# Kernel tuning notes

Measured on AMD Instinct MI355X. Metric: run time of the kernel, lower is better.

## Reference

```python
import jax, jax.numpy as jnp
import numpy as np

B, S, D, H = 4, 2048, 1024, 16
DH = D // H


def setup_inputs() -> dict:
    key = jax.random.key(0)
    ks = jax.random.split(key, 5)
    std = 1.0 / np.sqrt(D)
    return {
        "x": jax.random.normal(ks[0], (B, S, D), dtype=jnp.float32),
        "mask": jnp.ones((S, S), dtype=bool),  # unused by the original forward
        "Wq": jax.random.normal(ks[1], (D, D), dtype=jnp.float32) * std,
        "Wk": jax.random.normal(ks[2], (D, D), dtype=jnp.float32) * std,
        "Wv": jax.random.normal(ks[3], (D, D), dtype=jnp.float32) * std,
        "Wout": jax.random.normal(ks[4], (D, D), dtype=jnp.float32) * std,
    }


def reference(x, mask, Wq, Wk, Wv, Wout):
    n, s, d = x.shape
    scale = 1.0 / np.sqrt(DH).astype(np.float32)
    q = (x @ Wq).reshape(n, s, H, DH)
    k = (x @ Wk).reshape(n, s, H, DH)
    v = (x @ Wv).reshape(n, s, H, DH)
    # scores [n, q, k, h]; softmax over k axis (dim=-2 in original)
    attn = jnp.einsum('nqhd,nkhd->nqkh', q, k) * scale
    attn = jax.nn.softmax(attn, axis=-2)
    z = jnp.einsum('nqkh,nkhd->nqhd', attn, v).reshape(n, s, d)
    z = jnp.einsum('nqd,de->nqe', z, Wout)
    return x + z
```

## Files before the change

### kernel.cpp

```cpp
#include <hip/hip_runtime.h>

#define Bn 4
#define Sn 2048
#define Dn 1024
#define Hn 16
#define DHn 64

typedef float f32x4 __attribute__((ext_vector_type(4)));
typedef short bf16x8 __attribute__((ext_vector_type(8)));
typedef unsigned short u16;
typedef unsigned int u32;
typedef unsigned short u16x8 __attribute__((ext_vector_type(8)));
typedef unsigned short u16x4 __attribute__((ext_vector_type(4)));
typedef u32 u32x4 __attribute__((ext_vector_type(4)));

union B8 { u32x4 u; bf16x8 s; u16x8 h; };

__device__ __forceinline__ u16 f2bf(float f){
  union { float f; u32 u; } v; v.f = f;
  return (u16)((v.u + 0x7fffu + ((v.u >> 16) & 1u)) >> 16);
}

__device__ __forceinline__ u32 pack_bf2(float lo, float hi){
  union { float f; u32 u; } a, b;
  a.f = lo; b.f = hi;
  return __builtin_amdgcn_perm(b.u, a.u, 0x07060302u);
}

#if __has_builtin(__builtin_amdgcn_exp2f)
#define EXP2(x) __builtin_amdgcn_exp2f(x)
#define QSCALE 0.18033688011112042f
#else
#define EXP2(x) __expf(x)
#define QSCALE 0.125f
#endif

#if __has_builtin(__builtin_amdgcn_global_load_lds)
#define G2L16(l, g) __builtin_amdgcn_global_load_lds((const __attribute__((address_space(1))) u32*)(g), \
                                                     (__attribute__((address_space(3))) u32*)(l), 16, 0, 0)
#else
#define G2L16(l, g) (*(bf16x8*)(l) = *(const bf16x8*)(g))
#endif

#define MFMA_B16(d, va, vb) (d) = __builtin_amdgcn_mfma_f32_16x16x32_bf16((va), (vb), (d), 0, 0, 0)
#define BARRAW() __builtin_amdgcn_s_barrier()
#define WAIT_LGKM0() asm volatile("s_waitcnt lgkmcnt(0)" ::: "memory")
#define VM4() asm volatile("s_waitcnt vmcnt(4)" ::: "memory")
#define VM0() asm volatile("s_waitcnt vmcnt(0)" ::: "memory")
#define SCHEDB() __builtin_amdgcn_sched_barrier(0)

__global__ void prep_kernel(const float* __restrict__ x,
                            const float* __restrict__ Wq, const float* __restrict__ Wk,
                            const float* __restrict__ Wv, const float* __restrict__ Wo,
                            u16* __restrict__ xb, u16* __restrict__ wt_all){
  __shared__ u16 tile[64*66];
  const int t = threadIdx.x;
  if (blockIdx.x < 4096){
    size_t i = ((size_t)blockIdx.x * 256 + t) * 8;
    float4 f0 = *(const float4*)(x + i);
    float4 f1 = *(const float4*)(x + i + 4);
    u16x8 o;
    o[0]=f2bf(f0.x); o[1]=f2bf(f0.y); o[2]=f2bf(f0.z); o[3]=f2bf(f0.w);
    o[4]=f2bf(f1.x); o[5]=f2bf(f1.y); o[6]=f2bf(f1.z); o[7]=f2bf(f1.w);
    *(u16x8*)(xb + i) = o;
    return;
  }
  const int wi = blockIdx.x - 4096;
  const int z = wi >> 8, r8 = wi & 255;
  const int k0 = (r8 >> 4) * 64, n0 = (r8 & 15) * 64;
  const float* w = (z == 0) ? Wq : (z == 1) ? Wk : (z == 2) ? Wv : Wo;
  const float scale = (z == 0) ? QSCALE : 1.0f;
  u16* wt = wt_all + (size_t)z * Dn * Dn;
  #pragma unroll
  for (int i = 0; i < 4; i++){
    int idx = i*256 + t;
    int r = idx >> 4, c4 = (idx & 15) * 4;
    float4 f = *(const float4*)(w + (size_t)(k0 + r)*Dn + n0 + c4);
    tile[r*66 + c4 + 0] = f2bf(f.x * scale);
    tile[r*66 + c4 + 1] = f2bf(f.y * scale);
    tile[r*66 + c4 + 2] = f2bf(f.z * scale);
    tile[r*66 + c4 + 3] = f2bf(f.w * scale);
  }
  __syncthreads();
  #pragma unroll
  for (int i = 0; i < 4; i++){
    int idx = i*256 + t;
    int nr = idx >> 4, kc4 = (idx & 15) * 4;
    u16x4 o;
    o[0] = tile[(kc4+0)*66 + nr];
    o[1] = tile[(kc4+1)*66 + nr];
    o[2] = tile[(kc4+2)*66 + nr];
    o[3] = tile[(kc4+3)*66 + nr];
    *(u16x4*)(wt + (size_t)(n0 + nr)*Dn + k0 + kc4) = o;
  }
}

__launch_bounds__(256)
__global__ void gemm_qkv_kernel(const u16* __restrict__ xb, const u16* __restrict__ wt_all,
                                u16* __restrict__ qb, u16* __restrict__ kb, u16* __restrict__ vtb){
  __shared__ u16 sm[40960];
  const int t = threadIdx.x;
  const int lane = t & 63, wave = t >> 6;
  const int ln = lane & 15, quad = lane >> 4;
  const int wm = wave >> 1, wn = wave & 1;

  const int lin = blockIdx.x;
  const int wg = (lin & 7) * 192 + (lin >> 3);
  const int zsel = wg >> 9;
  const int rem = wg & 511;
  const int m0 = (rem >> 3) * 128;
  const int n0 = (rem & 7) * 128;
  const u16* wt = wt_all + (size_t)zsel * Dn * Dn;

  const u16* ap[4]; const u16* bp[4]; int ldo[4];
  #pragma unroll
  for (int p = 0; p < 4; p++){
    int idx = p*256 + t;
    int r = idx >> 3, g = (idx & 7) ^ (r & 7);
    ap[p] = xb + (size_t)(m0 + r)*Dn + g*8;
    bp[p] = wt + (size_t)(n0 + r)*Dn + g*8;
    ldo[p] = idx * 8;
  }
#define STGA(buf, tt) do { _Pragma("unroll") for (int p = 0; p < 4; p++) \
    G2L16(&sm[(buf) + ldo[p]], ap[p] + (size_t)(tt)*64); } while(0)
#define STGB(buf, tt) do { _Pragma("unroll") for (int p = 0; p < 4; p++) \
    G2L16(&sm[(buf) + ldo[p]], bp[p] + (size_t)(tt)*64); } while(0)

  const int agr0 = ((    quad) ^ (ln & 7)) * 8;
  const int agr1 = ((4 + quad) ^ (ln & 7)) * 8;
  int arow[4], brow[4];
  #pragma unroll
  for (int i = 0; i < 4; i++) arow[i] = (wm*64 + i*16 + ln) * 64;
  #pragma unroll
  for (int j = 0; j < 4; j++) brow[j] = (wn*64 + j*16 + ln) * 64;

  f32x4 acc[4][4] = {};

  STGA(0, 0); STGB(24576, 0); STGA(8192, 1);

  #pragma unroll
  for (int tt = 0; tt < 16; ++tt){
    const int a_cur = (tt % 3) * 8192;
    const int a_pf  = ((tt + 2) % 3) * 8192;
    const int b_cur = 24576 + (tt & 1) * 8192;
    const int b_pf  = 24576 + ((tt + 1) & 1) * 8192;

    if (tt < 15) { VM4(); } else { VM0(); }
    BARRAW(); SCHEDB();

    bf16x8 a01[2][2], bq[4][2];
    #pragma unroll
    for (int i = 0; i < 2; i++){
      a01[i][0] = *(const bf16x8*)&sm[a_cur + arow[i] + agr0];
      a01[i][1] = *(const bf16x8*)&sm[a_cur + arow[i] + agr1];
    }
    #pragma unroll
    for (int j = 0; j < 4; j++){
      bq[j][0] = *(const bf16x8*)&sm[b_cur + brow[j] + agr0];
      bq[j][1] = *(const bf16x8*)&sm[b_cur + brow[j] + agr1];
    }
    SCHEDB();
    if (tt < 15) STGB(b_pf, tt + 1);
    SCHEDB();
    WAIT_LGKM0(); SCHEDB();
    __builtin_amdgcn_s_setprio(1);
    #pragma unroll
    for (int i = 0; i < 2; i++)
      #pragma unroll
      for (int j = 0; j < 4; j++){
        MFMA_B16(acc[i][j], a01[i][0], bq[j][0]);
        MFMA_B16(acc[i][j], a01[i][1], bq[j][1]);
      }
    __builtin_amdgcn_s_setprio(0);

    bf16x8 a23[2][2];
    #pragma unroll
    for (int i = 0; i < 2; i++){
      a23[i][0] = *(const bf16x8*)&sm[a_cur + arow[2+i] + agr0];
      a23[i][1] = *(const bf16x8*)&sm[a_cur + arow[2+i] + agr1];
    }
    SCHEDB();
    if (tt < 14) STGA(a_pf, tt + 2);
    SCHEDB();
    WAIT_LGKM0(); SCHEDB();
    __builtin_amdgcn_s_setprio(1);
    #pragma unroll
    for (int i = 0; i < 2; i++)
      #pragma unroll
      for (int j = 0; j < 4; j++){
        MFMA_B16(acc[2+i][j], a23[i][0], bq[j][0]);
        MFMA_B16(acc[2+i][j], a23[i][1], bq[j][1]);
      }
    __builtin_amdgcn_s_setprio(0);
  }

  __syncthreads();
  u16* Cs = sm;
  if (zsel < 2){
    u16* outp = (zsel == 0) ? qb : kb;
    #pragma unroll
    for (int rb = 0; rb < 4; rb++)
      #pragma unroll
      for (int cb = 0; cb < 4; cb++)
        #pragma unroll
        for (int reg = 0; reg < 4; reg++)
          Cs[(wm*64 + rb*16 + quad*4 + reg)*136 + wn*64 + cb*16 + ln] = f2bf(acc[rb][cb][reg]);
    __syncthreads();
    #pragma unroll
    for (int i = 0; i < 8; i++){
      int idx = i*256 + t;
      int r = idx >> 4, c8 = (idx & 15) * 8;
      bf16x8 vdat = *(const bf16x8*)&Cs[r*136 + c8];
      int row = m0 + r, bb = row >> 11, s = row & 2047;
      int col = n0 + c8, hh = col >> 6, d = col & 63;
      *(bf16x8*)(outp + (((size_t)bb*Hn + hh)*Sn + s)*DHn + d) = vdat;
    }
  } else {
    #pragma unroll
    for (int rb = 0; rb < 4; rb++)
      #pragma unroll
      for (int cb = 0; cb < 4; cb++){
        u16x4 o;
        #pragma unroll
        for (int reg = 0; reg < 4; reg++) o[reg] = f2bf(acc[rb][cb][reg]);
        *(u16x4*)&Cs[(wn*64 + cb*16 + ln)*136 + wm*64 + rb*16 + quad*4] = o;
      }
    __syncthreads();
    #pragma unroll
    for (int i = 0; i < 8; i++){
      int idx = i*256 + t;
      int c = idx >> 4, r8 = (idx & 15) * 8;
      bf16x8 vdat = *(const bf16x8*)&Cs[c*136 + r8];
      int col = n0 + c, hh = col >> 6, d = col & 63;
      int row = m0 + r8, bb = row >> 11, s = row & 2047;
      *(bf16x8*)(vtb + (((size_t)bb*Hn + hh)*DHn + d)*Sn + s) = vdat;
    }
  }
#undef STGA
#undef STGB
}

__launch_bounds__(256, 2)
__global__ void attn_kernel(const u16* q, const u16* __restrict__ k,
                            const u16* __restrict__ vt, u16* z){
  __shared__ u16 Ks[2][64*72];
  __shared__ u16 Vs[2][64*72];
  const int t = threadIdx.x;
  const int wave = t >> 6, lane = t & 63;
  const int ln = lane & 15, quad = lane >> 4;
  const int lin = blockIdx.x + 8*(blockIdx.y + 16*blockIdx.z);
  const int wgs = (lin & 7)*64 + (lin >> 3);
  const int qt = wgs & 7, h = (wgs >> 3) & 15, b = wgs >> 7;
  const size_t bh = (size_t)b * Hn + h;
  const int q0 = qt*256 + wave*64;
  const u16* qp = q + bh * Sn * DHn;
  const u16* kp = k + bh * Sn * DHn;
  const u16* vp = vt + bh * DHn * Sn;

  bf16x8 qf[4][2];
  #pragma unroll
  for (int n = 0; n < 4; n++)
    #pragma unroll
    for (int kq = 0; kq < 2; kq++)
      qf[n][kq] = *(const bf16x8*)(qp + (size_t)(q0 + n*16 + ln)*DHn + kq*32 + quad*8);

  f32x4 zacc[4][4] = {};
  float dacc[4] = {0.f, 0.f, 0.f, 0.f};

  int sr[2], sc[2], vc1[2], vc2[2];
  #pragma unroll
  for (int i = 0; i < 2; i++){
    int idx = i*256 + t, r = idx >> 3, a = idx & 7;
    sr[i] = r; sc[i] = a*8;
    int ksg = a >> 2, q1 = ((a&3)*2)&3, h1 = (a&3) >> 1;
    vc1[i] = ksg*32 + q1*8 + h1*4;
    vc2[i] = ksg*32 + (((q1+1)&3))*8 + h1*4;
  }

  bf16x8 rk[2], rv[2];
  #pragma unroll
  for (int i = 0; i < 2; i++){
    rk[i] = *(const bf16x8*)(kp + (size_t)sr[i]*DHn + sc[i]);
    rv[i] = *(const bf16x8*)(vp + (size_t)sr[i]*Sn + sc[i]);
  }
  #pragma unroll
  for (int i = 0; i < 2; i++){
    *(bf16x8*)&Ks[0][sr[i]*72 + sc[i]] = rk[i];
    u16x4 lo = *(u16x4*)&rv[i];
    u16x4 hi = *((u16x4*)&rv[i] + 1);
    *(u16x4*)&Vs[0][sr[i]*72 + vc1[i]] = lo;
    *(u16x4*)&Vs[0][sr[i]*72 + vc2[i]] = hi;
  }

  for (int kt = 0; kt < Sn/64; kt++){
    const int cur = kt & 1;
    __syncthreads();

    if (kt + 1 < Sn/64){
      #pragma unroll
      for (int i = 0; i < 2; i++){
        rk[i] = *(const bf16x8*)(kp + (size_t)((kt+1)*64 + sr[i])*DHn + sc[i]);
        rv[i] = *(const bf16x8*)(vp + (size_t)sr[i]*Sn + (kt+1)*64 + sc[i]);
      }
    }
    const u16* Kc = Ks[cur];
    const u16* Vc = Vs[cur];

    #pragma unroll
    for (int ks = 0; ks < 2; ks++){
      f32x4 sacc[2][4] = {};
      #pragma unroll
      for (int kq = 0; kq < 2; kq++){
        bf16x8 ka[2];
        #pragma unroll
        for (int m2 = 0; m2 < 2; m2++)
          ka[m2] = *(const bf16x8*)&Kc[((2*ks + m2)*16 + ln)*72 + kq*32 + quad*8];
        #pragma unroll
        for (int m2 = 0; m2 < 2; m2++)
          #pragma unroll
          for (int n = 0; n < 4; n++)
            sacc[m2][n] = __builtin_amdgcn_mfma_f32_16x16x32_bf16(ka[m2], qf[n][kq], sacc[m2][n], 0, 0, 0);
      }
      B8 pb[4];
      #pragma unroll
      for (int n = 0; n < 4; n++){
        f32x4 s0 = sacc[0][n], s1 = sacc[1][n];
        float a0 = EXP2(s0[0]), a1 = EXP2(s0[1]), a2 = EXP2(s0[2]), a3 = EXP2(s0[3]);
        float b0 = EXP2(s1[0]), b1 = EXP2(s1[1]), b2 = EXP2(s1[2]), b3 = EXP2(s1[3]);
        dacc[n] += ((a0 + a1) + (a2 + a3)) + ((b0 + b1) + (b2 + b3));
        pb[n].u = (u32x4){pack_bf2(a0, a1), pack_bf2(a2, a3), pack_bf2(b0, b1), pack_bf2(b2, b3)};
      }
      #pragma unroll
      for (int mtd = 0; mtd < 4; mtd++){
        bf16x8 va = *(const bf16x8*)&Vc[(mtd*16 + ln)*72 + ks*32 + quad*8];
        #pragma unroll
        for (int n = 0; n < 4; n++)
          zacc[mtd][n] = __builtin_amdgcn_mfma_f32_16x16x32_bf16(va, pb[n].s, zacc[mtd][n], 0, 0, 0);
      }
    }

    if (kt + 1 < Sn/64){
      const int nxt = (kt+1) & 1;
      #pragma unroll
      for (int i = 0; i < 2; i++){
        *(bf16x8*)&Ks[nxt][sr[i]*72 + sc[i]] = rk[i];
        u16x4 lo = *(u16x4*)&rv[i];
        u16x4 hi = *((u16x4*)&rv[i] + 1);
        *(u16x4*)&Vs[nxt][sr[i]*72 + vc1[i]] = lo;
        *(u16x4*)&Vs[nxt][sr[i]*72 + vc2[i]] = hi;
      }
    }
  }

  float inv[4];
  #pragma unroll
  for (int n = 0; n < 4; n++){
    float d = dacc[n];
    d += __shfl_xor(d, 16, 64);
    d += __shfl_xor(d, 32, 64);
    inv[n] = 1.0f / d;
  }

  #pragma unroll
  for (int mtd = 0; mtd < 4; mtd++)
    #pragma unroll
    for (int n = 0; n < 4; n++){
      u16x4 o;
      #pragma unroll
      for (int j = 0; j < 4; j++) o[j] = f2bf(zacc[mtd][n][j] * inv[n]);
      *(u16x4*)(z + (bh*Sn + (size_t)(q0 + n*16 + ln))*DHn + mtd*16 + quad*4) = o;
    }
}

__launch_bounds__(256)
__global__ void gemm_out_kernel(const u16* __restrict__ zb, const u16* __restrict__ wt,
                                const float* __restrict__ x, float* __restrict__ out){
  __shared__ u16 sm[40960];
  const int t = threadIdx.x;
  const int lane = t & 63, wave = t >> 6;
  const int ln = lane & 15, quad = lane >> 4;
  const int wm = wave >> 1, wn = wave & 1;

  const int lin = blockIdx.x;
  const int wg = (lin & 7) * 64 + (lin >> 3);
  const int m0 = (wg >> 3) * 128;
  const int n0 = (wg & 7) * 128;

  const u16* ap[4]; const u16* bp[4]; int ldo[4];
  #pragma unroll
  for (int p = 0; p < 4; p++){
    int idx = p*256 + t;
    int r = idx >> 3, g = (idx & 7) ^ (r & 7);
    int row = m0 + r, bb = row >> 11, s = row & 2047;
    ap[p] = zb + ((size_t)bb*Hn*Sn + s)*DHn + g*8;
    bp[p] = wt + (size_t)(n0 + r)*Dn + g*8;
    ldo[p] = idx * 8;
  }
#define STGA(buf, tt) do { _Pragma("unroll") for (int p = 0; p < 4; p++) \
    G2L16(&sm[(buf) + ldo[p]], ap[p] + (size_t)(tt)*Sn*DHn); } while(0)
#define STGB(buf, tt) do { _Pragma("unroll") for (int p = 0; p < 4; p++) \
    G2L16(&sm[(buf) + ldo[p]], bp[p] + (size_t)(tt)*64); } while(0)

  const int agr0 = ((    quad) ^ (ln & 7)) * 8;
  const int agr1 = ((4 + quad) ^ (ln & 7)) * 8;
  int arow[4], brow[4];
  #pragma unroll
  for (int i = 0; i < 4; i++) arow[i] = (wm*64 + i*16 + ln) * 64;
  #pragma unroll
  for (int j = 0; j < 4; j++) brow[j] = (wn*64 + j*16 + ln) * 64;

  f32x4 acc[4][4] = {};
  STGA(0, 0); STGB(24576, 0); STGA(8192, 1);

  #pragma unroll
  for (int tt = 0; tt < 16; ++tt){
    const int a_cur = (tt % 3) * 8192;
    const int a_pf  = ((tt + 2) % 3) * 8192;
    const int b_cur = 24576 + (tt & 1) * 8192;
    const int b_pf  = 24576 + ((tt + 1) & 1) * 8192;

    if (tt < 15) { VM4(); } else { VM0(); }
    BARRAW(); SCHEDB();

    bf16x8 a01[2][2], bq[4][2];
    #pragma unroll
    for (int i = 0; i < 2; i++){
      a01[i][0] = *(const bf16x8*)&sm[a_cur + arow[i] + agr0];
      a01[i][1] = *(const bf16x8*)&sm[a_cur + arow[i] + agr1];
    }
    #pragma unroll
    for (int j = 0; j < 4; j++){
      bq[j][0] = *(const bf16x8*)&sm[b_cur + brow[j] + agr0];
      bq[j][1] = *(const bf16x8*)&sm[b_cur + brow[j] + agr1];
    }
    SCHEDB();
    if (tt < 15) STGB(b_pf, tt + 1);
    SCHEDB();
    WAIT_LGKM0(); SCHEDB();
    __builtin_amdgcn_s_setprio(1);
    #pragma unroll
    for (int i = 0; i < 2; i++)
      #pragma unroll
      for (int j = 0; j < 4; j++){
        MFMA_B16(acc[i][j], a01[i][0], bq[j][0]);
        MFMA_B16(acc[i][j], a01[i][1], bq[j][1]);
      }
    __builtin_amdgcn_s_setprio(0);

    bf16x8 a23[2][2];
    #pragma unroll
    for (int i = 0; i < 2; i++){
      a23[i][0] = *(const bf16x8*)&sm[a_cur + arow[2+i] + agr0];
      a23[i][1] = *(const bf16x8*)&sm[a_cur + arow[2+i] + agr1];
    }
    SCHEDB();
    if (tt < 14) STGA(a_pf, tt + 2);
    SCHEDB();
    WAIT_LGKM0(); SCHEDB();
    __builtin_amdgcn_s_setprio(1);
    #pragma unroll
    for (int i = 0; i < 2; i++)
      #pragma unroll
      for (int j = 0; j < 4; j++){
        MFMA_B16(acc[2+i][j], a23[i][0], bq[j][0]);
        MFMA_B16(acc[2+i][j], a23[i][1], bq[j][1]);
      }
    __builtin_amdgcn_s_setprio(0);
  }

  #pragma unroll
  for (int rb = 0; rb < 4; rb++)
    #pragma unroll
    for (int cb = 0; cb < 4; cb++)
      #pragma unroll
      for (int reg = 0; reg < 4; reg++){
        int row = m0 + wm*64 + rb*16 + quad*4 + reg;
        int col = n0 + wn*64 + cb*16 + ln;
        size_t off = (size_t)row*Dn + col;
        out[off] = acc[rb][cb][reg] + x[off];
      }
#undef STGA
#undef STGB
}

extern "C" void kernel_launch(void* const* d_in, const int* in_sizes, int n_in,
                              void* d_out, int out_size, void* d_ws, size_t ws_size,
                              hipStream_t stream){
  const float* x    = (const float*)d_in[0];
  const float* Wq   = (const float*)d_in[2];
  const float* Wk   = (const float*)d_in[3];
  const float* Wv   = (const float*)d_in[4];
  const float* Wout = (const float*)d_in[5];
  float* out = (float*)d_out;

  u16* ws = (u16*)d_ws;
  const size_t NW = (size_t)Dn * Dn;
  const size_t NX = (size_t)Bn * Sn * Dn;
  u16* wt  = ws;
  u16* xb  = wt + 4*NW;
  u16* qb  = xb + NX;
  u16* kb  = qb + NX;
  u16* vtb = kb + NX;

  prep_kernel     <<<dim3(4096 + 1024), dim3(256), 0, stream>>>(x, Wq, Wk, Wv, Wout, xb, wt);
  gemm_qkv_kernel <<<dim3(1536), dim3(256), 0, stream>>>(xb, wt, qb, kb, vtb);
  attn_kernel     <<<dim3(8,16,4), dim3(256), 0, stream>>>(qb, kb, vtb, qb);
  gemm_out_kernel <<<dim3(512), dim3(256), 0, stream>>>(qb, wt + 3*NW, x, out);
}
```

Before: 255.2 us.

## Use 8 waves of 32 query rows per attention block with XOR-swizzled LDS

The attention kernel now launches 512 threads per block, and each wave handles 32 query rows instead of 64. The per-wave accumulator and Q fragment register footprint is halved, and launch bounds now target higher occupancy. K/V tile staging is now one load per thread. LDS rows drop their 72-element padding in favour of an XOR swizzle on 8-element groups, which saves shared memory while still avoiding bank conflicts. In exchange, each wave now reuses every K/V fragment read from LDS across fewer MFMAs, and block-wide syncs cover more waves.

```diff
diff --git a/kernel.cpp b/kernel.cpp
--- a/kernel.cpp
+++ b/kernel.cpp
@@ -240,11 +240,11 @@
 #undef STGB
 }
 
-__launch_bounds__(256, 2)
+__launch_bounds__(512, 4)
 __global__ void attn_kernel(const u16* q, const u16* __restrict__ k,
                             const u16* __restrict__ vt, u16* z){
-  __shared__ u16 Ks[2][64*72];
-  __shared__ u16 Vs[2][64*72];
+  __shared__ u16 Ks[2][64*64];
+  __shared__ u16 Vs[2][64*64];
   const int t = threadIdx.x;
   const int wave = t >> 6, lane = t & 63;
   const int ln = lane & 15, quad = lane >> 4;
@@ -252,109 +252,102 @@
   const int wgs = (lin & 7)*64 + (lin >> 3);
   const int qt = wgs & 7, h = (wgs >> 3) & 15, b = wgs >> 7;
   const size_t bh = (size_t)b * Hn + h;
-  const int q0 = qt*256 + wave*64;
+  const int q0 = qt*256 + wave*32;
   const u16* qp = q + bh * Sn * DHn;
   const u16* kp = k + bh * Sn * DHn;
   const u16* vp = vt + bh * DHn * Sn;
 
-  bf16x8 qf[4][2];
-  #pragma unroll
-  for (int n = 0; n < 4; n++)
+  bf16x8 qf[2][2];
+  #pragma unroll
+  for (int n = 0; n < 2; n++)
     #pragma unroll
     for (int kq = 0; kq < 2; kq++)
       qf[n][kq] = *(const bf16x8*)(qp + (size_t)(q0 + n*16 + ln)*DHn + kq*32 + quad*8);
 
-  f32x4 zacc[4][4] = {};
-  float dacc[4] = {0.f, 0.f, 0.f, 0.f};
-
-  int sr[2], sc[2], vc1[2], vc2[2];
-  #pragma unroll
-  for (int i = 0; i < 2; i++){
-    int idx = i*256 + t, r = idx >> 3, a = idx & 7;
-    sr[i] = r; sc[i] = a*8;
-    int ksg = a >> 2, q1 = ((a&3)*2)&3, h1 = (a&3) >> 1;
-    vc1[i] = ksg*32 + q1*8 + h1*4;
-    vc2[i] = ksg*32 + (((q1+1)&3))*8 + h1*4;
-  }
-
-  bf16x8 rk[2], rv[2];
-  #pragma unroll
-  for (int i = 0; i < 2; i++){
-    rk[i] = *(const bf16x8*)(kp + (size_t)sr[i]*DHn + sc[i]);
-    rv[i] = *(const bf16x8*)(vp + (size_t)sr[i]*Sn + sc[i]);
-  }
-  #pragma unroll
-  for (int i = 0; i < 2; i++){
-    *(bf16x8*)&Ks[0][sr[i]*72 + sc[i]] = rk[i];
-    u16x4 lo = *(u16x4*)&rv[i];
-    u16x4 hi = *((u16x4*)&rv[i] + 1);
-    *(u16x4*)&Vs[0][sr[i]*72 + vc1[i]] = lo;
-    *(u16x4*)&Vs[0][sr[i]*72 + vc2[i]] = hi;
-  }
+  f32x4 zacc[4][2] = {};
+  float dacc[2] = {0.f, 0.f};
+
+  const int r = t >> 3, a = t & 7;
+  const int ksg = a >> 2, q1 = ((a&3)*2)&3, h1 = (a&3) >> 1;
+  const int vc1 = ksg*32 + q1*8 + h1*4;
+  const int vc2 = ksg*32 + (((q1+1)&3))*8 + h1*4;
+  const int kpos  = r*64 + (a ^ (r&7))*8;
+  const int vpos1 = r*64 + ((vc1>>3) ^ (r&7))*8 + (vc1 & 7);
+  const int vpos2 = r*64 + ((vc2>>3) ^ (r&7))*8 + (vc2 & 7);
+
+  bf16x8 rk, rv;
+  rk = *(const bf16x8*)(kp + (size_t)r*DHn + a*8);
+  rv = *(const bf16x8*)(vp + (size_t)r*Sn + a*8);
+  {
+    *(bf16x8*)&Ks[0][kpos] = rk;
+    u16x4 lo = *(u16x4*)&rv;
+    u16x4 hi = *((u16x4*)&rv + 1);
+    *(u16x4*)&Vs[0][vpos1] = lo;
+    *(u16x4*)&Vs[0][vpos2] = hi;
+  }
+
+  const int kg0 = ((    quad) ^ (ln & 7)) * 8;
+  const int kg1 = ((4 + quad) ^ (ln & 7)) * 8;
 
   for (int kt = 0; kt < Sn/64; kt++){
     const int cur = kt & 1;
     __syncthreads();
 
     if (kt + 1 < Sn/64){
-      #pragma unroll
-      for (int i = 0; i < 2; i++){
-        rk[i] = *(const bf16x8*)(kp + (size_t)((kt+1)*64 + sr[i])*DHn + sc[i]);
-        rv[i] = *(const bf16x8*)(vp + (size_t)sr[i]*Sn + (kt+1)*64 + sc[i]);
-      }
+      rk = *(const bf16x8*)(kp + (size_t)((kt+1)*64 + r)*DHn + a*8);
+      rv = *(const bf16x8*)(vp + (size_t)r*Sn + (kt+1)*64 + a*8);
     }
     const u16* Kc = Ks[cur];
     const u16* Vc = Vs[cur];
 
     #pragma unroll
     for (int ks = 0; ks < 2; ks++){
-      f32x4 sacc[2][4] = {};
+      f32x4 sacc[2][2] = {};
       #pragma unroll
       for (int kq = 0; kq < 2; kq++){
+        const int kgo = kq ? kg1 : kg0;
         bf16x8 ka[2];
         #pragma unroll
         for (int m2 = 0; m2 < 2; m2++)
-          ka[m2] = *(const bf16x8*)&Kc[((2*ks + m2)*16 + ln)*72 + kq*32 + quad*8];
+          ka[m2] = *(const bf16x8*)&Kc[((2*ks + m2)*16 + ln)*64 + kgo];
         #pragma unroll
         for (int m2 = 0; m2 < 2; m2++)
           #pragma unroll
-          for (int n = 0; n < 4; n++)
+          for (int n = 0; n < 2; n++)
             sacc[m2][n] = __builtin_amdgcn_mfma_f32_16x16x32_bf16(ka[m2], qf[n][kq], sacc[m2][n], 0, 0, 0);
       }
-      B8 pb[4];
-      #pragma unroll
-      for (int n = 0; n < 4; n++){
+      B8 pb[2];
+      #pragma unroll
+      for (int n = 0; n < 2; n++){
         f32x4 s0 = sacc[0][n], s1 = sacc[1][n];
         float a0 = EXP2(s0[0]), a1 = EXP2(s0[1]), a2 = EXP2(s0[2]), a3 = EXP2(s0[3]);
         float b0 = EXP2(s1[0]), b1 = EXP2(s1[1]), b2 = EXP2(s1[2]), b3 = EXP2(s1[3]);
         dacc[n] += ((a0 + a1) + (a2 + a3)) + ((b0 + b1) + (b2 + b3));
         pb[n].u = (u32x4){pack_bf2(a0, a1), pack_bf2(a2, a3), pack_bf2(b0, b1), pack_bf2(b2, b3)};
       }
+      const int vgo = ks ? kg1 : kg0;
       #pragma unroll
       for (int mtd = 0; mtd < 4; mtd++){
-        bf16x8 va = *(const bf16x8*)&Vc[(mtd*16 + ln)*72 + ks*32 + quad*8];
+        bf16x8 va = *(const bf16x8*)&Vc[(mtd*16 + ln)*64 + vgo];
         #pragma unroll
-        for (int n = 0; n < 4; n++)
+        for (int n = 0; n < 2; n++)
           zacc[mtd][n] = __builtin_amdgcn_mfma_f32_16x16x32_bf16(va, pb[n].s, zacc[mtd][n], 0, 0, 0);
       }
     }
 
     if (kt + 1 < Sn/64){
       const int nxt = (kt+1) & 1;
-      #pragma unroll
-      for (int i = 0; i < 2; i++){
-        *(bf16x8*)&Ks[nxt][sr[i]*72 + sc[i]] = rk[i];
-        u16x4 lo = *(u16x4*)&rv[i];
-        u16x4 hi = *((u16x4*)&rv[i] + 1);
-        *(u16x4*)&Vs[nxt][sr[i]*72 + vc1[i]] = lo;
-        *(u16x4*)&Vs[nxt][sr[i]*72 + vc2[i]] = hi;
-      }
-    }
-  }
-
-  float inv[4];
-  #pragma unroll
-  for (int n = 0; n < 4; n++){
+      *(bf16x8*)&Ks[nxt][kpos] = rk;
+      u16x4 lo = *(u16x4*)&rv;
+      u16x4 hi = *((u16x4*)&rv + 1);
+      *(u16x4*)&Vs[nxt][vpos1] = lo;
+      *(u16x4*)&Vs[nxt][vpos2] = hi;
+    }
+  }
+
+  float inv[2];
+  #pragma unroll
+  for (int n = 0; n < 2; n++){
     float d = dacc[n];
     d += __shfl_xor(d, 16, 64);
     d += __shfl_xor(d, 32, 64);
@@ -364,7 +357,7 @@
   #pragma unroll
   for (int mtd = 0; mtd < 4; mtd++)
     #pragma unroll
-    for (int n = 0; n < 4; n++){
+    for (int n = 0; n < 2; n++){
       u16x4 o;
       #pragma unroll
       for (int j = 0; j < 4; j++) o[j] = f2bf(zacc[mtd][n][j] * inv[n]);
@@ -504,6 +497,6 @@
 
   prep_kernel     <<<dim3(4096 + 1024), dim3(256), 0, stream>>>(x, Wq, Wk, Wv, Wout, xb, wt);
   gemm_qkv_kernel <<<dim3(1536), dim3(256), 0, stream>>>(xb, wt, qb, kb, vtb);
-  attn_kernel     <<<dim3(8,16,4), dim3(256), 0, stream>>>(qb, kb, vtb, qb);
+  attn_kernel     <<<dim3(8,16,4), dim3(512), 0, stream>>>(qb, kb, vtb, qb);
   gemm_out_kernel <<<dim3(512), dim3(256), 0, stream>>>(qb, wt + 3*NW, x, out);
 }
```

Measured after the change: 252.9 us. About the same (-0.9%).
